# Optimization experiments

Hardware: AMD Instinct MI355X
Metric: run time of the kernel (lower is better)

The kernel has to match this reference:

```python
import jax, jax.numpy as jnp
import numpy as np
from jax import lax

_EPS = 1e-6
N_POINTS = 2048


def quat_to_rot(q):
    # q = (x, y, z, w), same convention as quaternion_to_rotation_matrix_torch
    # (its analytic Jacobians dR/dq in the kernel match this unnormalized form)
    x, y, z, w = q[0], q[1], q[2], q[3]
    return jnp.stack([
        jnp.stack([1 - 2 * (y * y + z * z), 2 * (x * y - z * w), 2 * (x * z + y * w)]),
        jnp.stack([2 * (x * y + z * w), 1 - 2 * (x * x + z * z), 2 * (y * z - x * w)]),
        jnp.stack([2 * (x * z - y * w), 2 * (y * z + x * w), 1 - 2 * (x * x + y * y)]),
    ])


def setup_inputs() -> dict:
    key = jax.random.key(0)
    ks = jax.random.split(key, 8)
    H, W = 512, 512
    # points in front of camera, projecting inside the image
    z = jax.random.uniform(ks[0], (N_POINTS, 1), minval=2.0, maxval=6.0)
    xy_dir = jax.random.uniform(ks[1], (N_POINTS, 2), minval=-0.45, maxval=0.45)
    pointcloud = jnp.concatenate([xy_dir * z, z], axis=1)  # [N,3]
    point_color = jax.random.uniform(ks[2], (N_POINTS, 3))
    point_alpha = jax.random.uniform(ks[3], (N_POINTS,), minval=0.1, maxval=0.9)
    # conic = inverse 2x2 covariance in pixel space, stored (a, b, c):
    ac = jax.random.uniform(ks[4], (N_POINTS, 2), minval=0.02, maxval=0.10)
    b = jax.random.uniform(ks[5], (N_POINTS, 1), minval=-0.01, maxval=0.01)
    point_conic = jnp.concatenate([ac[:, :1], b, ac[:, 1:]], axis=1)  # [N,3]
    # near-identity camera pose (x,y,z,w quaternion)
    q = jnp.array([0.01, -0.02, 0.015, 1.0], dtype=jnp.float32)
    q_pointcloud_camera = q / jnp.linalg.norm(q)
    t_pointcloud_camera = 0.05 * jax.random.normal(ks[6], (3,), dtype=jnp.float32)
    fx = fy = 500.0
    camera_intrinsics = jnp.array([[fx, 0.0, W / 2.0], [0.0, fy, H / 2.0], [0.0, 0.0, 1.0]], dtype=jnp.float32)
    return {
        "pointcloud": pointcloud.astype(jnp.float32),
        "point_color": point_color.astype(jnp.float32),
        "point_alpha": point_alpha.astype(jnp.float32),
        "point_conic": point_conic.astype(jnp.float32),
        "q_pointcloud_camera": q_pointcloud_camera,
        "t_pointcloud_camera": t_pointcloud_camera,
        "camera_intrinsics": camera_intrinsics,
        "camera_height": H,
        "camera_width": W,
    }


def _rasterize(pointcloud, point_color, point_alpha, point_conic, q, t, K, H, W):
    R = quat_to_rot(q)
    p_cam = pointcloud @ R.T + t  # [N,3] camera-frame positions
    depth = p_cam[:, 2]
    proj = p_cam @ K.T
    uv = proj[:, :2] / (depth[:, None] + _EPS)  # [N,2] pixel coords
    # depth sort (front-to-back), matching the sorted per-tile traversal
    order = jnp.argsort(depth)
    uv_s = uv[order]
    conic_s = point_conic[order]
    col_s = point_color[order]
    a_s = point_alpha[order]
    d_s = depth[order]

    px = jnp.arange(W, dtype=jnp.float32) + 0.5  # pixel centers, as in kernel
    py = jnp.arange(H, dtype=jnp.float32) + 0.5

    def step(carry, xs):
        T, rgb, dacc = carry
        uv_i, conic_i, col_i, a_i, d_i = xs
        dx = px[None, :] - uv_i[0]  # [1,W] -> broadcast [H,W]
        dy = py[:, None] - uv_i[1]  # [H,1]
        power = -0.5 * (conic_i[0] * dx * dx + 2.0 * conic_i[1] * dx * dy + conic_i[2] * dy * dy)
        g = jnp.exp(jnp.minimum(power, 0.0))  # gaussian density in [0,1]
        prod = g * a_i
        alpha = jnp.where(prod >= 1.0 / 255.0, jnp.minimum(prod, 0.99), 0.0)
        w = T * alpha
        rgb = rgb + w[..., None] * col_i
        dacc = dacc + w * d_i
        T = T * (1.0 - alpha)
        return (T, rgb, dacc), None

    carry0 = (jnp.ones((H, W), jnp.float32), jnp.zeros((H, W, 3), jnp.float32), jnp.zeros((H, W), jnp.float32))
    (T, rgb, dacc), _ = lax.scan(step, carry0, (uv_s, conic_s, col_s, a_s, d_s))
    # [H,W,5] = rgb, rasterized_depth, accumulated_alpha
    return jnp.concatenate([rgb, dacc[..., None], (1.0 - T)[..., None]], axis=-1)


def reference(pointcloud, point_color, point_alpha, point_conic, q_pointcloud_camera, t_pointcloud_camera, camera_intrinsics, camera_height, camera_width):
    return _rasterize(pointcloud, point_color, point_alpha, point_conic,
                      q_pointcloud_camera, t_pointcloud_camera, camera_intrinsics,
                      camera_height, camera_width)
```

## Files before the change

kernel.cpp:

```cpp
#include <hip/hip_runtime.h>
#include <math.h>

#define NPTS 2048
#define IMG_W 512
#define IMG_H 512
#define RW 32
#define RH 16
#define NBX (IMG_W / RW)
#define NBY (IMG_H / RH)
#define NTHREADS (RW * RH)
#define NCHUNK (NPTS / NTHREADS)
#define CAP 512
#define RSTRIDE 12

__global__ __launch_bounds__(NTHREADS) void gs_fused(
    const float* __restrict__ pc,
    const float* __restrict__ col,
    const float* __restrict__ alp,
    const float* __restrict__ con,
    const float* __restrict__ q,
    const float* __restrict__ t,
    const float* __restrict__ K,
    float* __restrict__ out) {
  __shared__ float s_pts[CAP * RSTRIDE];
  __shared__ unsigned long long s_key[CAP];
  __shared__ int s_order[CAP];
  __shared__ int s_cnt[NCHUNK * 8];

  int tid = threadIdx.x;
  int lane = tid & 63, wave = tid >> 6;
  int rx = (blockIdx.x % NBX) * RW;
  int ry = (blockIdx.x / NBX) * RH;
  int lx = tid % RW, ly = tid / RW;
  float px = rx + lx + 0.5f, py = ry + ly + 0.5f;
  float tx0 = rx + 0.5f, tx1 = rx + RW - 0.5f;
  float ty0 = ry + 0.5f, ty1 = ry + RH - 0.5f;

  float qx = q[0], qy = q[1], qz = q[2], qw = q[3];
  float r00 = 1.f - 2.f * (qy * qy + qz * qz), r01 = 2.f * (qx * qy - qz * qw),
        r02 = 2.f * (qx * qz + qy * qw);
  float r10 = 2.f * (qx * qy + qz * qw), r11 = 1.f - 2.f * (qx * qx + qz * qz),
        r12 = 2.f * (qy * qz - qx * qw);
  float r20 = 2.f * (qx * qz - qy * qw), r21 = 2.f * (qy * qz + qx * qw),
        r22 = 1.f - 2.f * (qx * qx + qy * qy);
  float t0 = t[0], t1 = t[1], t2 = t[2];
  float fx = K[0], cx = K[2], fy = K[4], cy = K[5];

#define PROJ(i, ux, uy, Z)                      \
  float ux, uy, Z;                              \
  {                                             \
    float x = pc[3 * (i)], y = pc[3 * (i) + 1], \
          z = pc[3 * (i) + 2];                  \
    Z = r20 * x + r21 * y + r22 * z + t2;       \
    float X = r00 * x + r01 * y + r02 * z + t0; \
    float Y = r10 * x + r11 * y + r12 * z + t1; \
    float inv = 1.0f / (Z + 1e-6f);             \
    ux = (fx * X + cx * Z) * inv;               \
    uy = (fy * Y + cy * Z) * inv;               \
  }

  unsigned pmask = 0;
  int miw[NCHUNK];
#pragma unroll
  for (int c = 0; c < NCHUNK; c++) {
    int i = c * NTHREADS + tid;
    PROJ(i, ux, uy, Z);
    float A = con[3 * i], B = con[3 * i + 1], C = con[3 * i + 2];
    float a = alp[i];
    float th = 2.0f * __logf(255.0f * a);
    float absB = fabsf(B);
    float dxm = fmaxf(0.0f, fmaxf(tx0 - ux, ux - tx1));
    float dym = fmaxf(0.0f, fmaxf(ty0 - uy, uy - ty1));
    float bound =
        fmaxf(A - absB, 0.0f) * dxm * dxm + fmaxf(C - absB, 0.0f) * dym * dym;
    bool pred = bound <= th + 1e-3f;
    unsigned long long m = __ballot(pred);
    miw[c] = __popcll(m & ((1ull << lane) - 1ull));
    if (lane == 0) s_cnt[c * 8 + wave] = (int)__popcll(m);
    pmask |= (unsigned)pred << c;
  }
  __syncthreads();

  int start[NCHUNK], total;
  {
    int run = 0;
#pragma unroll
    for (int c = 0; c < NCHUNK; c++) {
      int woff = 0, ct = 0;
#pragma unroll
      for (int w = 0; w < 8; w++) {
        int v = s_cnt[c * 8 + w];
        woff += (w < wave) ? v : 0;
        ct += v;
      }
      start[c] = run + woff;
      run += ct;
    }
    total = run;
  }

  float T = 1.0f, accr = 0.f, accg = 0.f, accb = 0.f, accd = 0.f;

#define COMPOSITE(w0, w1, w2)                                              \
  {                                                                        \
    float dx = px - w0.x, dy = py - w0.y;                                  \
    float pw =                                                             \
        -0.5f * (w0.z * dx * dx + 2.0f * w0.w * dx * dy + w1.x * dy * dy); \
    float gg = __expf(fminf(pw, 0.0f));                                    \
    float prod = gg * w1.y;                                                \
    if (prod >= (1.0f / 255.0f)) {                                         \
      float al = fminf(prod, 0.99f);                                       \
      float w = T * al;                                                    \
      accr += w * w2.x;                                                    \
      accg += w * w2.y;                                                    \
      accb += w * w2.z;                                                    \
      accd += w * w1.z;                                                    \
      T *= (1.0f - al);                                                    \
    }                                                                      \
  }

  if (total <= CAP) {
#pragma unroll
    for (int c = 0; c < NCHUNK; c++) {
      if ((pmask >> c) & 1) {
        int i = c * NTHREADS + tid;
        PROJ(i, ux, uy, Z);
        float a = alp[i];
        float th = 2.0f * __logf(255.0f * a);
        int slot = start[c] + miw[c];
        float4* d = (float4*)(s_pts + (size_t)slot * RSTRIDE);
        d[0] = {ux, uy, con[3 * i], con[3 * i + 1]};
        d[1] = {con[3 * i + 2], a, Z, th};
        d[2] = {col[3 * i], col[3 * i + 1], col[3 * i + 2], 0.0f};
        s_key[slot] =
            ((unsigned long long)__float_as_uint(Z) << 32) | (unsigned)i;
      }
    }
    __syncthreads();

    if (tid < total) {
      unsigned long long myk = s_key[tid];
      int pos = 0;
      for (int j = 0; j < total; j++) pos += (s_key[j] < myk);
      s_order[pos] = tid;
    }
    __syncthreads();

    for (int kk = 0; kk < total; kk++) {
      int e = s_order[kk];
      const float4* p4 = (const float4*)(s_pts + (size_t)e * RSTRIDE);
      float4 w0 = p4[0], w1 = p4[1], w2 = p4[2];
      COMPOSITE(w0, w1, w2);
    }
  } else {
    float dep[NCHUNK];
#pragma unroll
    for (int c = 0; c < NCHUNK; c++) {
      int i = c * NTHREADS + tid;
      float x = pc[3 * i], y = pc[3 * i + 1], z = pc[3 * i + 2];
      dep[c] = r20 * x + r21 * y + r22 * z + t2;
    }
    unsigned live = pmask;
    float* s_rd = s_pts;
    int* s_ro = (int*)(s_pts + NTHREADS);
    float* s_rec = s_pts + 2 * NTHREADS;
    while (1) {
      float bd = 1e30f;
      int bo = 0x7fffffff;
#pragma unroll
      for (int c = 0; c < NCHUNK; c++) {
        if ((live >> c) & 1) {
          int o = c * NTHREADS + tid;
          if (dep[c] < bd || (dep[c] == bd && o < bo)) { bd = dep[c]; bo = o; }
        }
      }
      s_rd[tid] = bd;
      s_ro[tid] = bo;
      __syncthreads();
      float wd = 1e30f;
      int wo = 0x7fffffff;
      for (int j = 0; j < NTHREADS; j++) {
        float d = s_rd[j];
        int o = s_ro[j];
        if (d < wd || (d == wd && o < wo)) { wd = d; wo = o; }
      }
      __syncthreads();
      if (wo == 0x7fffffff) break;
      if (tid == (wo & (NTHREADS - 1))) {
        int i = wo;
        PROJ(i, ux, uy, Z);
        float a = alp[i];
        float4* d = (float4*)s_rec;
        d[0] = {ux, uy, con[3 * i], con[3 * i + 1]};
        d[1] = {con[3 * i + 2], a, Z, 0.0f};
        d[2] = {col[3 * i], col[3 * i + 1], col[3 * i + 2], 0.0f};
        live &= ~(1u << (wo / NTHREADS));
      }
      __syncthreads();
      float4 w0 = ((float4*)s_rec)[0], w1 = ((float4*)s_rec)[1],
             w2 = ((float4*)s_rec)[2];
      COMPOSITE(w0, w1, w2);
    }
  }
#undef COMPOSITE
#undef PROJ

  int o = ((ry + ly) * IMG_W + (rx + lx)) * 5;
  out[o + 0] = accr;
  out[o + 1] = accg;
  out[o + 2] = accb;
  out[o + 3] = accd;
  out[o + 4] = 1.0f - T;
}

extern "C" void kernel_launch(void* const* d_in, const int* in_sizes, int n_in,
                              void* d_out, int out_size, void* d_ws,
                              size_t ws_size, hipStream_t stream) {
  const float* pc = (const float*)d_in[0];
  const float* col = (const float*)d_in[1];
  const float* alp = (const float*)d_in[2];
  const float* con = (const float*)d_in[3];
  const float* q = (const float*)d_in[4];
  const float* t = (const float*)d_in[5];
  const float* K = (const float*)d_in[6];
  float* out = (float*)d_out;

  gs_fused<<<NBX * NBY, NTHREADS, 0, stream>>>(pc, col, alp, con, q, t, K,
                                               out);
}
```

Baseline: 18.38 us.

## Composite two pixel rows per thread on 32x32 tiles and sort records in place

```diff
diff --git a/kernel.cpp b/kernel.cpp
--- a/kernel.cpp
+++ b/kernel.cpp
@@ -5,10 +5,10 @@
 #define IMG_W 512
 #define IMG_H 512
 #define RW 32
-#define RH 16
+#define RH 32
 #define NBX (IMG_W / RW)
 #define NBY (IMG_H / RH)
-#define NTHREADS (RW * RH)
+#define NTHREADS 512
 #define NCHUNK (NPTS / NTHREADS)
 #define CAP 512
 #define RSTRIDE 12
@@ -24,15 +24,15 @@
     float* __restrict__ out) {
   __shared__ float s_pts[CAP * RSTRIDE];
   __shared__ unsigned long long s_key[CAP];
-  __shared__ int s_order[CAP];
   __shared__ int s_cnt[NCHUNK * 8];
 
   int tid = threadIdx.x;
   int lane = tid & 63, wave = tid >> 6;
   int rx = (blockIdx.x % NBX) * RW;
   int ry = (blockIdx.x / NBX) * RH;
-  int lx = tid % RW, ly = tid / RW;
-  float px = rx + lx + 0.5f, py = ry + ly + 0.5f;
+  int lx = tid & 31, ly = tid >> 5;
+  float px = rx + lx + 0.5f;
+  float py0 = ry + ly + 0.5f;
   float tx0 = rx + 0.5f, tx1 = rx + RW - 0.5f;
   float ty0 = ry + 0.5f, ty1 = ry + RH - 0.5f;
 
@@ -99,24 +99,34 @@
     total = run;
   }
 
-  float T = 1.0f, accr = 0.f, accg = 0.f, accb = 0.f, accd = 0.f;
-
-#define COMPOSITE(w0, w1, w2)                                              \
-  {                                                                        \
-    float dx = px - w0.x, dy = py - w0.y;                                  \
-    float pw =                                                             \
-        -0.5f * (w0.z * dx * dx + 2.0f * w0.w * dx * dy + w1.x * dy * dy); \
-    float gg = __expf(fminf(pw, 0.0f));                                    \
-    float prod = gg * w1.y;                                                \
-    if (prod >= (1.0f / 255.0f)) {                                         \
-      float al = fminf(prod, 0.99f);                                       \
-      float w = T * al;                                                    \
-      accr += w * w2.x;                                                    \
-      accg += w * w2.y;                                                    \
-      accb += w * w2.z;                                                    \
-      accd += w * w1.z;                                                    \
-      T *= (1.0f - al);                                                    \
-    }                                                                      \
+  float T0 = 1.0f, ar0 = 0.f, ag0 = 0.f, ab0 = 0.f, ad0 = 0.f;
+  float T1 = 1.0f, ar1 = 0.f, ag1 = 0.f, ab1 = 0.f, ad1 = 0.f;
+
+#define COMPOSITE2(w0, w1, w2)                                   \
+  {                                                              \
+    float dx = px - w0.x;                                        \
+    float dy0 = py0 - w0.y, dy1 = dy0 + 16.0f;                   \
+    float adx2 = w0.z * dx * dx;                                 \
+    float bdx2 = 2.0f * w0.w * dx;                               \
+    float pw0 = -0.5f * (adx2 + bdx2 * dy0 + w1.x * dy0 * dy0);  \
+    float pw1 = -0.5f * (adx2 + bdx2 * dy1 + w1.x * dy1 * dy1);  \
+    float g0 = __expf(fminf(pw0, 0.0f));                         \
+    float g1 = __expf(fminf(pw1, 0.0f));                         \
+    float prod0 = g0 * w1.y, prod1 = g1 * w1.y;                  \
+    if (prod0 >= (1.0f / 255.0f)) {                              \
+      float al = fminf(prod0, 0.99f);                            \
+      float w = T0 * al;                                         \
+      ar0 += w * w2.x; ag0 += w * w2.y; ab0 += w * w2.z;         \
+      ad0 += w * w1.z;                                           \
+      T0 *= (1.0f - al);                                         \
+    }                                                            \
+    if (prod1 >= (1.0f / 255.0f)) {                              \
+      float al = fminf(prod1, 0.99f);                            \
+      float w = T1 * al;                                         \
+      ar1 += w * w2.x; ag1 += w * w2.y; ab1 += w * w2.z;         \
+      ad1 += w * w1.z;                                           \
+      T1 *= (1.0f - al);                                         \
+    }                                                            \
   }
 
   if (total <= CAP) {
@@ -138,19 +148,27 @@
     }
     __syncthreads();
 
-    if (tid < total) {
-      unsigned long long myk = s_key[tid];
-      int pos = 0;
+    bool have = tid < total;
+    unsigned long long myk = 0;
+    float4 ra, rb, rc;
+    int pos = 0;
+    if (have) {
+      myk = s_key[tid];
+      const float4* s = (const float4*)(s_pts + (size_t)tid * RSTRIDE);
+      ra = s[0]; rb = s[1]; rc = s[2];
       for (int j = 0; j < total; j++) pos += (s_key[j] < myk);
-      s_order[pos] = tid;
     }
     __syncthreads();
+    if (have) {
+      float4* d = (float4*)(s_pts + (size_t)pos * RSTRIDE);
+      d[0] = ra; d[1] = rb; d[2] = rc;
+    }
+    __syncthreads();
 
     for (int kk = 0; kk < total; kk++) {
-      int e = s_order[kk];
-      const float4* p4 = (const float4*)(s_pts + (size_t)e * RSTRIDE);
+      const float4* p4 = (const float4*)(s_pts + (size_t)kk * RSTRIDE);
       float4 w0 = p4[0], w1 = p4[1], w2 = p4[2];
-      COMPOSITE(w0, w1, w2);
+      COMPOSITE2(w0, w1, w2);
     }
   } else {
     float dep[NCHUNK];
@@ -199,18 +217,24 @@
       __syncthreads();
       float4 w0 = ((float4*)s_rec)[0], w1 = ((float4*)s_rec)[1],
              w2 = ((float4*)s_rec)[2];
-      COMPOSITE(w0, w1, w2);
-    }
-  }
-#undef COMPOSITE
+      COMPOSITE2(w0, w1, w2);
+    }
+  }
+#undef COMPOSITE2
 #undef PROJ
 
-  int o = ((ry + ly) * IMG_W + (rx + lx)) * 5;
-  out[o + 0] = accr;
-  out[o + 1] = accg;
-  out[o + 2] = accb;
-  out[o + 3] = accd;
-  out[o + 4] = 1.0f - T;
+  int o0 = ((ry + ly) * IMG_W + (rx + lx)) * 5;
+  int o1 = ((ry + ly + 16) * IMG_W + (rx + lx)) * 5;
+  out[o0 + 0] = ar0;
+  out[o0 + 1] = ag0;
+  out[o0 + 2] = ab0;
+  out[o0 + 3] = ad0;
+  out[o0 + 4] = 1.0f - T0;
+  out[o1 + 0] = ar1;
+  out[o1 + 1] = ag1;
+  out[o1 + 2] = ab1;
+  out[o1 + 3] = ad1;
+  out[o1 + 4] = 1.0f - T1;
 }
 
 extern "C" void kernel_launch(void* const* d_in, const int* in_sizes, int n_in,
```

New measurement: 19.73 us. 1.07x slower.

## Shrink tiles to 16x16 and physically reorder splat records after rank sort

Applied to the files above, without the earlier changes.

```diff
diff --git a/kernel.cpp b/kernel.cpp
--- a/kernel.cpp
+++ b/kernel.cpp
@@ -4,13 +4,14 @@
 #define NPTS 2048
 #define IMG_W 512
 #define IMG_H 512
-#define RW 32
+#define RW 16
 #define RH 16
 #define NBX (IMG_W / RW)
 #define NBY (IMG_H / RH)
-#define NTHREADS (RW * RH)
+#define NTHREADS 256
+#define NWAVES (NTHREADS / 64)
 #define NCHUNK (NPTS / NTHREADS)
-#define CAP 512
+#define CAP 256
 #define RSTRIDE 12
 
 __global__ __launch_bounds__(NTHREADS) void gs_fused(
@@ -24,15 +25,15 @@
     float* __restrict__ out) {
   __shared__ float s_pts[CAP * RSTRIDE];
   __shared__ unsigned long long s_key[CAP];
-  __shared__ int s_order[CAP];
-  __shared__ int s_cnt[NCHUNK * 8];
+  __shared__ int s_cnt[NCHUNK * NWAVES];
 
   int tid = threadIdx.x;
   int lane = tid & 63, wave = tid >> 6;
   int rx = (blockIdx.x % NBX) * RW;
   int ry = (blockIdx.x / NBX) * RH;
-  int lx = tid % RW, ly = tid / RW;
-  float px = rx + lx + 0.5f, py = ry + ly + 0.5f;
+  int lx = tid & 15, ly = tid >> 4;
+  float px = rx + lx + 0.5f;
+  float py = ry + ly + 0.5f;
   float tx0 = rx + 0.5f, tx1 = rx + RW - 0.5f;
   float ty0 = ry + 0.5f, ty1 = ry + RH - 0.5f;
 
@@ -76,7 +77,7 @@
     bool pred = bound <= th + 1e-3f;
     unsigned long long m = __ballot(pred);
     miw[c] = __popcll(m & ((1ull << lane) - 1ull));
-    if (lane == 0) s_cnt[c * 8 + wave] = (int)__popcll(m);
+    if (lane == 0) s_cnt[c * NWAVES + wave] = (int)__popcll(m);
     pmask |= (unsigned)pred << c;
   }
   __syncthreads();
@@ -88,8 +89,8 @@
     for (int c = 0; c < NCHUNK; c++) {
       int woff = 0, ct = 0;
 #pragma unroll
-      for (int w = 0; w < 8; w++) {
-        int v = s_cnt[c * 8 + w];
+      for (int w = 0; w < NWAVES; w++) {
+        int v = s_cnt[c * NWAVES + w];
         woff += (w < wave) ? v : 0;
         ct += v;
       }
@@ -138,17 +139,25 @@
     }
     __syncthreads();
 
-    if (tid < total) {
-      unsigned long long myk = s_key[tid];
-      int pos = 0;
+    bool have = tid < total;
+    unsigned long long myk = 0;
+    float4 ra, rb, rc;
+    int pos = 0;
+    if (have) {
+      myk = s_key[tid];
+      const float4* s = (const float4*)(s_pts + (size_t)tid * RSTRIDE);
+      ra = s[0]; rb = s[1]; rc = s[2];
       for (int j = 0; j < total; j++) pos += (s_key[j] < myk);
-      s_order[pos] = tid;
     }
     __syncthreads();
+    if (have) {
+      float4* d = (float4*)(s_pts + (size_t)pos * RSTRIDE);
+      d[0] = ra; d[1] = rb; d[2] = rc;
+    }
+    __syncthreads();
 
     for (int kk = 0; kk < total; kk++) {
-      int e = s_order[kk];
-      const float4* p4 = (const float4*)(s_pts + (size_t)e * RSTRIDE);
+      const float4* p4 = (const float4*)(s_pts + (size_t)kk * RSTRIDE);
       float4 w0 = p4[0], w1 = p4[1], w2 = p4[2];
       COMPOSITE(w0, w1, w2);
     }
```

New measurement: 19.14 us. 4.1% more time.
